# Kernel optimization log

Hardware: AMD Instinct MI355X
Metric: run time of the kernel (lower is better)

The kernel has to match this reference:

```python
import jax, jax.numpy as jnp
import numpy as np

S, B, D_MODEL, H, DH = 2048, 2, 1024, 16, 64
FACTOR = 1.0 / np.sqrt(DH).astype(np.float32)


def setup_inputs() -> dict:
    key = jax.random.key(0)
    ks = jax.random.split(key, 12)
    sc = 0.02
    inp = {
        'query': jax.random.normal(ks[0], (S, B, D_MODEL), jnp.float32),
        'key': jax.random.normal(ks[1], (S, B, D_MODEL), jnp.float32),
        'value': jax.random.normal(ks[2], (S, B, D_MODEL), jnp.float32),
        # causal mask [seq_q, seq_k, 1]; 0 -> masked
        'mask': jnp.tril(jnp.ones((S, S), dtype=bool))[:, :, None],
        'Wq': jax.random.normal(ks[3], (H * DH, D_MODEL), jnp.float32) * sc,
        'bq': jnp.zeros((H * DH,), jnp.float32),
        'Wk': jax.random.normal(ks[4], (H * DH, D_MODEL), jnp.float32) * sc,
        'bk': jnp.zeros((H * DH,), jnp.float32),
        'Wv': jax.random.normal(ks[5], (H * DH, D_MODEL), jnp.float32) * sc,
        'bv': jnp.zeros((H * DH,), jnp.float32),
        'Wo': jax.random.normal(ks[6], (D_MODEL, H * DH), jnp.float32) * sc,
        'bo': jnp.zeros((D_MODEL,), jnp.float32),
    }
    return inp


def _split_heads(x):
    # pattern: 's b (head_dim head_num) -> s b head_num head_dim' (head_dim is OUTER)
    s, b, _ = x.shape
    return x.reshape(s, b, DH, H).transpose(0, 1, 3, 2)  # [s,b,H,DH]


def reference(query, key, value, mask, Wq, bq, Wk, bk, Wv, bv, Wo, bo):
    q = _split_heads(query @ Wq.T + bq)
    k = _split_heads(key @ Wk.T + bk)
    v = _split_heads(value @ Wv.T + bv)
    scores = jnp.einsum('ibhd,jbhd->ijbh', q, k) * FACTOR  # [i,j,b,h]
    scores = jnp.where(mask[..., None], scores, -jnp.inf)
    attn = jax.nn.softmax(scores, axis=1)  # softmax over keys (dim=1)
    out = jnp.einsum('ijbh,jbhd->ibhd', attn, v)  # [i,b,h,d]
    out = out.reshape(S, B, H * DH)  # 'i b h d -> i b (h d)'
    return out @ Wo.T + bo
```

## Files before the change

kernel.cpp:

```cpp
#include <hip/hip_runtime.h>


typedef float f32x4 __attribute__((ext_vector_type(4)));
typedef float f32x16 __attribute__((ext_vector_type(16)));
typedef __bf16 bf16x8_t __attribute__((ext_vector_type(8)));
typedef unsigned short ushort8 __attribute__((ext_vector_type(8)));
typedef unsigned int uint4v __attribute__((ext_vector_type(4)));
typedef unsigned int uint2v __attribute__((ext_vector_type(2)));

#define S_LEN 2048
#define BATCH 2
#define DMODEL 1024
#define NHEAD 16
#define DHEAD 64
#define K_SCALE 0.18033688011112042f
#define NCHUNK 51

__device__ __forceinline__ unsigned short f2bf(float x) {
  unsigned int u = __builtin_bit_cast(unsigned int, x);
  u += 0x7fffu + ((u >> 16) & 1u);
  return (unsigned short)(u >> 16);
}

__device__ __forceinline__ f32x4 mfma16(ushort8 a, ushort8 b, f32x4 c) {
  return __builtin_amdgcn_mfma_f32_16x16x32_bf16(
      __builtin_bit_cast(bf16x8_t, a), __builtin_bit_cast(bf16x8_t, b), c, 0, 0, 0);
}
__device__ __forceinline__ f32x16 mfma32(ushort8 a, ushort8 b, f32x16 c) {
  return __builtin_amdgcn_mfma_f32_32x32x16_bf16(
      __builtin_bit_cast(bf16x8_t, a), __builtin_bit_cast(bf16x8_t, b), c, 0, 0, 0);
}

__device__ __forceinline__ float max3f(float a, float b, float c) {
  return fmaxf(fmaxf(a, b), c);
}

__device__ __forceinline__ ushort8 pack8(float4 a, float4 b, float s) {
  ushort8 t;
  t[0] = f2bf(a.x * s); t[1] = f2bf(a.y * s); t[2] = f2bf(a.z * s); t[3] = f2bf(a.w * s);
  t[4] = f2bf(b.x * s); t[5] = f2bf(b.y * s); t[6] = f2bf(b.z * s); t[7] = f2bf(b.w * s);
  return t;
}

__device__ __forceinline__ void gload16(unsigned short* lds, const unsigned short* g) {
  __builtin_amdgcn_global_load_lds(
      (const __attribute__((address_space(1))) unsigned int*)g,
      (__attribute__((address_space(3))) unsigned int*)lds, 16, 0, 0);
}

__global__ __launch_bounds__(256) void cvt_kernel(
    const float* __restrict__ q, const float* __restrict__ k, const float* __restrict__ v,
    const float* __restrict__ wq, const float* __restrict__ wk,
    const float* __restrict__ wv, const float* __restrict__ wo,
    unsigned short* __restrict__ qB, unsigned short* __restrict__ kB,
    unsigned short* __restrict__ vB, unsigned short* __restrict__ wqB,
    unsigned short* __restrict__ wkB, unsigned short* __restrict__ wvB,
    unsigned short* __restrict__ woB)
{
  const int c = blockIdx.x * 256 + threadIdx.x;
  const float* s; unsigned short* d; int base;
  if      (c < 524288)  { s = q;  d = qB;  base = 0; }
  else if (c < 1048576) { s = k;  d = kB;  base = 524288; }
  else if (c < 1572864) { s = v;  d = vB;  base = 1048576; }
  else if (c < 1703936) { s = wq; d = wqB; base = 1572864; }
  else if (c < 1835008) { s = wk; d = wkB; base = 1703936; }
  else if (c < 1966080) { s = wv; d = wvB; base = 1835008; }
  else                  { s = wo; d = woB; base = 1966080; }
  const size_t off = (size_t)(c - base) * 8;
  const float4 v0 = *reinterpret_cast<const float4*>(s + off);
  const float4 v1 = *reinterpret_cast<const float4*>(s + off + 4);
  *reinterpret_cast<ushort8*>(d + off) = pack8(v0, v1, 1.0f);
}

__global__ __launch_bounds__(256) void gemm_qkv_kernel(
    const unsigned short* __restrict__ qA, const unsigned short* __restrict__ kA,
    const unsigned short* __restrict__ vA,
    const unsigned short* __restrict__ wqW, const unsigned short* __restrict__ wkW,
    const unsigned short* __restrict__ wvW,
    const float* __restrict__ bq, const float* __restrict__ bk,
    const float* __restrict__ bv,
    unsigned short* __restrict__ Cq, unsigned short* __restrict__ Ck,
    unsigned short* __restrict__ Cv)
{
  __shared__ __align__(16) unsigned short As[2][128 * 64];
  __shared__ __align__(16) unsigned short Ws[2][64 * 64];
  const int z = blockIdx.z;
  const unsigned short* A = (z == 0) ? qA : (z == 1) ? kA : vA;
  const unsigned short* W = (z == 0) ? wqW : (z == 1) ? wkW : wvW;
  const float* bias = (z == 0) ? bq : (z == 1) ? bk : bv;
  unsigned short* C = (z == 0) ? Cq : (z == 1) ? Ck : Cv;
  const float oscale = (z == 1) ? K_SCALE : 1.0f;

  const int tid = threadIdx.x;
  const int lane = tid & 63;
  const int w = tid >> 6;
  const int wm = (w >> 1) * 64, wn = (w & 1) * 32;
  const int g = lane >> 4, lr = lane & 15;

  const int bid = (int)blockIdx.x;
  const int widx = (bid & 7) * 64 + (bid >> 3);
  const int n0 = (widx & 15) * 64;
  const int m0 = (widx >> 4) * 128;

  f32x4 acc[4][2] = {};

#define STAGE(buf, k0)                                                              \
  {                                                                                 \
    _Pragma("unroll")                                                               \
    for (int ii = 0; ii < 4; ++ii) {                                                \
      const int c = ii * 256 + tid;                                                 \
      const int row = c >> 3;                                                       \
      const int sl = (c & 7) ^ (row & 7);                                           \
      gload16(&As[buf][c * 8], A + (size_t)(m0 + row) * DMODEL + (k0) + sl * 8);    \
    }                                                                               \
    _Pragma("unroll")                                                               \
    for (int ii = 0; ii < 2; ++ii) {                                                \
      const int c = ii * 256 + tid;                                                 \
      const int row = c >> 3;                                                       \
      const int sl = (c & 7) ^ (row & 7);                                           \
      gload16(&Ws[buf][c * 8], W + (size_t)(n0 + row) * DMODEL + (k0) + sl * 8);    \
    }                                                                               \
  }

  STAGE(0, 0);
  int cur = 0;

  for (int t = 0; t < 16; ++t) {
    __syncthreads();
    if (t < 15) STAGE(cur ^ 1, (t + 1) * 64);

    const char* ab = (const char*)&As[cur][0];
    const char* wb = (const char*)&Ws[cur][0];
#pragma unroll
    for (int kk = 0; kk < 2; ++kk) {
      ushort8 af[4], bw[2];
#pragma unroll
      for (int mt = 0; mt < 4; ++mt) {
        const int row = wm + mt * 16 + lr;
        af[mt] = *reinterpret_cast<const ushort8*>(
            ab + row * 128 + (((kk * 4 + g) ^ (row & 7)) << 4));
      }
#pragma unroll
      for (int nt = 0; nt < 2; ++nt) {
        const int row = wn + nt * 16 + lr;
        bw[nt] = *reinterpret_cast<const ushort8*>(
            wb + row * 128 + (((kk * 4 + g) ^ (row & 7)) << 4));
      }
      __builtin_amdgcn_s_setprio(1);
#pragma unroll
      for (int mt = 0; mt < 4; ++mt)
#pragma unroll
        for (int nt = 0; nt < 2; ++nt)
          acc[mt][nt] = mfma16(af[mt], bw[nt], acc[mt][nt]);
      __builtin_amdgcn_s_setprio(0);
    }
    cur ^= 1;
  }
#undef STAGE

#pragma unroll
  for (int nt = 0; nt < 2; ++nt) {
    const int col = n0 + wn + nt * 16 + lr;
    const float bvv = bias[col];
#pragma unroll
    for (int mt = 0; mt < 4; ++mt)
#pragma unroll
      for (int r = 0; r < 4; ++r) {
        const int rowg = m0 + wm + mt * 16 + g * 4 + r;
        C[(size_t)rowg * DMODEL + col] = f2bf((acc[mt][nt][r] + bvv) * oscale);
      }
  }
}

__global__ __launch_bounds__(256) void gemm_out_kernel(
    const unsigned short* __restrict__ A, const unsigned short* __restrict__ W,
    const float* __restrict__ bias, float* __restrict__ C)
{
  __shared__ __align__(16) unsigned short As[2][128 * 64];
  __shared__ __align__(16) unsigned short Ws[2][64 * 64];
  const int tid = threadIdx.x;
  const int lane = tid & 63;
  const int w = tid >> 6;
  const int wm = (w >> 1) * 64, wn = (w & 1) * 32;
  const int g = lane >> 4, lr = lane & 15;

  const int bid = (int)blockIdx.x;
  const int widx = (bid & 7) * 64 + (bid >> 3);
  const int n0 = (widx & 15) * 64;
  const int m0 = (widx >> 4) * 128;

  f32x4 acc[4][2] = {};

#define STAGE(buf, k0)                                                              \
  {                                                                                 \
    _Pragma("unroll")                                                               \
    for (int ii = 0; ii < 4; ++ii) {                                                \
      const int c = ii * 256 + tid;                                                 \
      const int row = c >> 3;                                                       \
      const int sl = (c & 7) ^ (row & 7);                                           \
      gload16(&As[buf][c * 8], A + (size_t)(m0 + row) * DMODEL + (k0) + sl * 8);    \
    }                                                                               \
    _Pragma("unroll")                                                               \
    for (int ii = 0; ii < 2; ++ii) {                                                \
      const int c = ii * 256 + tid;                                                 \
      const int row = c >> 3;                                                       \
      const int sl = (c & 7) ^ (row & 7);                                           \
      gload16(&Ws[buf][c * 8], W + (size_t)(n0 + row) * DMODEL + (k0) + sl * 8);    \
    }                                                                               \
  }

  STAGE(0, 0);
  int cur = 0;

  for (int t = 0; t < 16; ++t) {
    __syncthreads();
    if (t < 15) STAGE(cur ^ 1, (t + 1) * 64);

    const char* ab = (const char*)&As[cur][0];
    const char* wb = (const char*)&Ws[cur][0];
#pragma unroll
    for (int kk = 0; kk < 2; ++kk) {
      ushort8 af[4], bw[2];
#pragma unroll
      for (int mt = 0; mt < 4; ++mt) {
        const int row = wm + mt * 16 + lr;
        af[mt] = *reinterpret_cast<const ushort8*>(
            ab + row * 128 + (((kk * 4 + g) ^ (row & 7)) << 4));
      }
#pragma unroll
      for (int nt = 0; nt < 2; ++nt) {
        const int row = wn + nt * 16 + lr;
        bw[nt] = *reinterpret_cast<const ushort8*>(
            wb + row * 128 + (((kk * 4 + g) ^ (row & 7)) << 4));
      }
      __builtin_amdgcn_s_setprio(1);
#pragma unroll
      for (int mt = 0; mt < 4; ++mt)
#pragma unroll
        for (int nt = 0; nt < 2; ++nt)
          acc[mt][nt] = mfma16(af[mt], bw[nt], acc[mt][nt]);
      __builtin_amdgcn_s_setprio(0);
    }
    cur ^= 1;
  }
#undef STAGE

#pragma unroll
  for (int nt = 0; nt < 2; ++nt) {
    const int col = n0 + wn + nt * 16 + lr;
    const float bvv = bias[col];
#pragma unroll
    for (int mt = 0; mt < 4; ++mt)
#pragma unroll
      for (int r = 0; r < 4; ++r) {
        const int rowg = m0 + wm + mt * 16 + g * 4 + r;
        C[(size_t)rowg * DMODEL + col] = acc[mt][nt][r] + bvv;
      }
  }
}

__global__ __launch_bounds__(256) void transpose_all_kernel(
    const unsigned short* __restrict__ in0, unsigned short* __restrict__ out0,
    const unsigned short* __restrict__ in1, unsigned short* __restrict__ out1,
    const unsigned short* __restrict__ in2, unsigned short* __restrict__ out2)
{
  __shared__ __align__(16) unsigned short T[32 * 256];
  const int bx = (int)blockIdx.x;
  const int tid = threadIdx.x;

  if (bx < 1024) {
    const unsigned short* in = (bx < 512) ? in0 : in1;
    unsigned short* out = (bx < 512) ? out0 : out1;
    const int lb = bx & 511;
    const int n0 = (lb & 127) * 32, o0 = (lb >> 7) * 256;
#pragma unroll
    for (int i = 0; i < 4; ++i) {
      const int c = i * 256 + tid;
      const int row = c >> 5, c8 = c & 31;
      ushort8 v = *reinterpret_cast<const ushort8*>(in + (size_t)(n0 + row) * DMODEL + o0 + c8 * 8);
      int y = (row * 512 + c8 * 16) ^ ((row & 3) << 5);
      *reinterpret_cast<ushort8*>((char*)T + y) = v;
    }
    __syncthreads();
    const int d0 = o0 >> 4, s0 = n0 >> 1;
#pragma unroll
    for (int rep = 0; rep < 2; ++rep) {
      const int e = rep * 256 + tid;
      const int hh = e & 15, s = (e >> 4) & 15, b = (e >> 8) & 1;
      const int n = s * 2 + b;
      unsigned short vals[16];
#pragma unroll
      for (int dd = 0; dd < 16; ++dd) {
        int y = n * 512 + ((dd * 32 + hh * 2) ^ ((n & 3) << 5));
        vals[dd] = *(const unsigned short*)((const char*)T + y);
      }
      uint4v w0, w1;
#pragma unroll
      for (int j = 0; j < 4; ++j) {
        w0[j] = (unsigned)vals[2 * j] | ((unsigned)vals[2 * j + 1] << 16);
        w1[j] = (unsigned)vals[8 + 2 * j] | ((unsigned)vals[8 + 2 * j + 1] << 16);
      }
      unsigned short* dst = out + ((size_t)(b * 16 + hh) * S_LEN + s0 + s) * DHEAD + d0;
      *reinterpret_cast<uint4v*>(dst) = w0;
      *reinterpret_cast<uint4v*>(dst + 8) = w1;
    }
  } else {
    const int lb = bx - 1024;
    const int n0 = (lb & 63) * 64, o0 = (lb >> 6) * 64;
#pragma unroll
    for (int i = 0; i < 2; ++i) {
      const int c = i * 256 + tid;
      const int row = c >> 3, c8 = c & 7;
      ushort8 v = *reinterpret_cast<const ushort8*>(in2 + (size_t)(n0 + row) * DMODEL + o0 + c8 * 8);
      int y = (row * 128 + c8 * 16) ^ ((row & 7) << 4);
      *reinterpret_cast<ushort8*>((char*)T + y) = v;
    }
    __syncthreads();
    const int d0 = o0 >> 4, s0 = n0 >> 1;
    const int shalf = tid & 1, seg = tid >> 1;
    const int dd = seg & 3, hh = (seg >> 2) & 15, b = (seg >> 6) & 1;
    unsigned short vals[16];
#pragma unroll
    for (int i = 0; i < 16; ++i) {
      const int s = shalf * 16 + i;
      const int n = s * 2 + b;
      int y = n * 128 + (((dd * 16 + hh) * 2) ^ ((n & 7) << 4));
      vals[i] = *(const unsigned short*)((const char*)T + y);
    }
    uint4v w0, w1;
#pragma unroll
    for (int j = 0; j < 4; ++j) {
      w0[j] = (unsigned)vals[2 * j] | ((unsigned)vals[2 * j + 1] << 16);
      w1[j] = (unsigned)vals[8 + 2 * j] | ((unsigned)vals[8 + 2 * j + 1] << 16);
    }
    unsigned short* dst = out2 + ((size_t)(b * 16 + hh) * DHEAD + d0 + dd) * S_LEN + s0 + shalf * 16;
    *reinterpret_cast<uint4v*>(dst) = w0;
    *reinterpret_cast<uint4v*>(dst + 8) = w1;
  }
}

__global__ __launch_bounds__(256, 4) void attn_part_kernel(
    const unsigned short* __restrict__ Qh, const unsigned short* __restrict__ Kh,
    const unsigned short* __restrict__ Vh, unsigned short* __restrict__ Opart,
    float* __restrict__ mlbuf)
{
  __shared__ __align__(16) unsigned short Ks[2][64 * 64];
  __shared__ __align__(16) unsigned short Vs[2][64 * 64];

  const int tid = threadIdx.x;
  const int lane = tid & 63;
  const int w = tid >> 6;
  const int ln31 = lane & 31;
  const int hf = lane >> 5;

  const int bid = (int)blockIdx.x;
  const int xcd = bid & 7;
  const int sl8 = bid >> 3;
  const int hb = xcd * 4 + sl8 / NCHUNK;
  const int chunkid = sl8 % NCHUNK;

  int u = chunkid;
  int Q = 0, nc = 1;
  while (u >= nc) { u -= nc; ++Q; nc = Q / 3 + 1; }
  const int c = u;

  const int head = hb & 15, b = hb >> 4;
  const int slot = hb * NCHUNK + chunkid;
  const int t0 = c * 6;
  const int tmax = 2 * Q + 1;
  const int t1 = (tmax < t0 + 5) ? tmax : (t0 + 5);
  const int q0 = Q * 128;

  const size_t hoff = (size_t)(b * NHEAD + head) * (S_LEN * DHEAD);
  const unsigned short* Qg = Qh + hoff;
  const unsigned short* Kg = Kh + hoff;
  const unsigned short* Vg = Vh + hoff;

  const int qwb = q0 + w * 32;
  const int qg = qwb + ln31;

  ushort8 qf[4];
#pragma unroll
  for (int kt = 0; kt < 4; ++kt)
    qf[kt] = *reinterpret_cast<const ushort8*>(Qg + (size_t)qg * DHEAD + kt * 16 + hf * 8);

  f32x16 oa0 = {0}, oa1 = {0};
  float mrun = -1e30f, ssum = 0.f;

#define STAGE(buf, kv)                                                             \
  {                                                                                \
    _Pragma("unroll")                                                              \
    for (int ii = 0; ii < 2; ++ii) {                                               \
      const int c2 = ii * 256 + tid;                                               \
      const int row = c2 >> 3;                                                     \
      const int sl = (c2 & 7) ^ (row & 7);                                         \
      gload16(&Ks[buf][c2 * 8], Kg + (size_t)((kv) + row) * 64 + sl * 8);          \
    }                                                                              \
    _Pragma("unroll")                                                              \
    for (int ii = 0; ii < 2; ++ii) {                                               \
      const int c2 = ii * 256 + tid;                                               \
      const int row = c2 >> 3;                                                     \
      const int sl = (c2 & 7) ^ (row & 7);                                         \
      gload16(&Vs[buf][c2 * 8], Vg + (size_t)row * S_LEN + (kv) + sl * 8);         \
    }                                                                              \
  }

  STAGE(0, t0 * 64);
  int cur = 0;

  const int kb0 = ln31 * 128 + ((hf * 16) ^ ((ln31 & 7) << 4));
  const int kb1 = (32 + ln31) * 128 + ((hf * 16) ^ ((ln31 & 7) << 4));

  for (int t = t0; t <= t1; ++t) {
    const int kv0 = t * 64;
    __syncthreads();
    if (t < t1) STAGE(cur ^ 1, kv0 + 64);

    if (kv0 <= qwb + 31) {
      f32x16 sc0 = {0}, sc1 = {0};
      {
        const char* ksb = (const char*)&Ks[cur][0];
        __builtin_amdgcn_s_setprio(1);
#pragma unroll
        for (int kt = 0; kt < 4; ++kt) {
          ushort8 kf0 = *reinterpret_cast<const ushort8*>(ksb + (kb0 ^ (kt << 5)));
          ushort8 kf1 = *reinterpret_cast<const ushort8*>(ksb + (kb1 ^ (kt << 5)));
          sc0 = mfma32(kf0, qf[kt], sc0);
          sc1 = mfma32(kf1, qf[kt], sc1);
        }
        __builtin_amdgcn_s_setprio(0);
      }

      if (kv0 + 63 > qwb) {
#pragma unroll
        for (int r = 0; r < 16; ++r) {
          const int keyb = kv0 + (r & 3) + 8 * (r >> 2) + 4 * hf;
          if (keyb > qg) sc0[r] = -1e30f;
          if (keyb + 32 > qg) sc1[r] = -1e30f;
        }
      }

      float m0a = max3f(sc0[0], sc0[1], sc0[2]);
      float m1a = max3f(sc0[3], sc0[4], sc0[5]);
      float m2a = max3f(sc0[6], sc0[7], sc0[8]);
      float m3a = max3f(sc0[9], sc0[10], sc0[11]);
      float m4a = max3f(sc0[12], sc0[13], sc0[14]);
      float m5a = max3f(sc0[15], sc1[0], sc1[1]);
      float m6a = max3f(sc1[2], sc1[3], sc1[4]);
      float m7a = max3f(sc1[5], sc1[6], sc1[7]);
      float m8a = max3f(sc1[8], sc1[9], sc1[10]);
      float m9a = max3f(sc1[11], sc1[12], sc1[13]);
      float mAa = fmaxf(sc1[14], sc1[15]);
      float n0a = max3f(m0a, m1a, m2a);
      float n1a = max3f(m3a, m4a, m5a);
      float n2a = max3f(m6a, m7a, m8a);
      float n3a = fmaxf(m9a, mAa);
      float pmax = fmaxf(max3f(n0a, n1a, n2a), n3a);
      pmax = fmaxf(pmax, __shfl_xor(pmax, 32, 64));

      if (!__all(pmax <= mrun + 8.0f)) {
        const float mnew = fmaxf(mrun, pmax);
        const float scl = exp2f(mrun - mnew);
        ssum *= scl;
#pragma unroll
        for (int r = 0; r < 16; ++r) { oa0[r] *= scl; oa1[r] *= scl; }
        mrun = mnew;
      }

      float pv0[16], pv1[16];
#pragma unroll
      for (int r = 0; r < 16; ++r) {
        pv0[r] = exp2f(sc0[r] - mrun);
        pv1[r] = exp2f(sc1[r] - mrun);
      }
      float a8[8];
#pragma unroll
      for (int r = 0; r < 8; ++r)
        a8[r] = (pv0[r] + pv0[r + 8]) + (pv1[r] + pv1[r + 8]);
      float a4_0 = a8[0] + a8[4], a4_1 = a8[1] + a8[5];
      float a4_2 = a8[2] + a8[6], a4_3 = a8[3] + a8[7];
      float psum = (a4_0 + a4_1) + (a4_2 + a4_3);
      psum += __shfl_xor(psum, 32, 64);
      ssum += psum;

      unsigned int cc[16];
#pragma unroll
      for (int j = 0; j < 8; ++j) {
        asm("v_cvt_pk_bf16_f32 %0, %1, %2" : "=v"(cc[j]) : "v"(pv0[2 * j]), "v"(pv0[2 * j + 1]));
        asm("v_cvt_pk_bf16_f32 %0, %1, %2" : "=v"(cc[8 + j]) : "v"(pv1[2 * j]), "v"(pv1[2 * j + 1]));
      }

      uint4v pfw[4];
#pragma unroll
      for (int mt = 0; mt < 2; ++mt) {
#pragma unroll
        for (int ktl = 0; ktl < 2; ++ktl) {
          const int o = mt * 8 + ktl * 4;
          unsigned x0 = cc[o + 0], x2 = cc[o + 2];
          unsigned y0 = cc[o + 1], y2 = cc[o + 3];
          asm("v_permlane32_swap_b32 %0, %1" : "+v"(x0), "+v"(x2));
          asm("v_permlane32_swap_b32 %0, %1" : "+v"(y0), "+v"(y2));
          uint4v u4;
          u4[0] = x0; u4[1] = y0; u4[2] = x2; u4[3] = y2;
          pfw[mt * 2 + ktl] = u4;
        }
      }

      {
        const char* vsb = (const char*)&Vs[cur][0];
        __builtin_amdgcn_s_setprio(1);
#pragma unroll
        for (int kt = 0; kt < 4; ++kt) {
          ushort8 vf0 = *reinterpret_cast<const ushort8*>(vsb + (kb0 ^ (kt << 5)));
          ushort8 vf1 = *reinterpret_cast<const ushort8*>(vsb + (kb1 ^ (kt << 5)));
          ushort8 pfr = __builtin_bit_cast(ushort8, pfw[kt]);
          oa0 = mfma32(vf0, pfr, oa0);
          oa1 = mfma32(vf1, pfr, oa1);
        }
        __builtin_amdgcn_s_setprio(0);
      }
    }

    cur ^= 1;
  }
#undef STAGE

  const int ql = w * 32 + ln31;
  unsigned short* ob = Opart + (size_t)slot * 8192 + ql * 64;
#pragma unroll
  for (int mt2 = 0; mt2 < 2; ++mt2) {
#pragma unroll
    for (int rq = 0; rq < 4; ++rq) {
      const int dd = mt2 * 32 + 8 * rq + 4 * hf;
      const f32x16& a = mt2 ? oa1 : oa0;
      unsigned int w0, w1;
      asm("v_cvt_pk_bf16_f32 %0, %1, %2" : "=v"(w0)
          : "v"(a[4 * rq + 0]), "v"(a[4 * rq + 1]));
      asm("v_cvt_pk_bf16_f32 %0, %1, %2" : "=v"(w1)
          : "v"(a[4 * rq + 2]), "v"(a[4 * rq + 3]));
      uint2v pk = { w0, w1 };
      *reinterpret_cast<uint2v*>(ob + dd) = pk;
    }
  }
  if (hf == 0) {
    mlbuf[slot * 256 + ql] = mrun;
    mlbuf[slot * 256 + 128 + ql] = ssum;
  }
}

__global__ __launch_bounds__(256) void attn_combine_kernel(
    const unsigned short* __restrict__ Opart, const float* __restrict__ mlbuf,
    unsigned short* __restrict__ O)
{
  const int Q = blockIdx.x, hb = blockIdx.y;
  const int head = hb & 15, b = hb >> 4;
  const int nch = Q / 3 + 1;
  int off = 0;
  for (int j = 0; j < Q; ++j) off += j / 3 + 1;
  const int s0 = hb * NCHUNK + off;

  const int tid = threadIdx.x;
  const int q = tid >> 1, dh = (tid & 1) * 32;

  float mc[6], lc[6];
  float M = -1e30f;
  for (int cc = 0; cc < nch; ++cc) {
    mc[cc] = mlbuf[(s0 + cc) * 256 + q];
    lc[cc] = mlbuf[(s0 + cc) * 256 + 128 + q];
    M = fmaxf(M, mc[cc]);
  }
  float L = 0.f, wgt[6];
  for (int cc = 0; cc < nch; ++cc) {
    wgt[cc] = exp2f(mc[cc] - M);
    L += wgt[cc] * lc[cc];
  }
  const float invL = 1.0f / L;

  float acc[32] = {};
  for (int cc = 0; cc < nch; ++cc) {
    const unsigned short* p = Opart + (size_t)(s0 + cc) * 8192 + q * 64 + dh;
    const float wv = wgt[cc];
#pragma unroll
    for (int seg = 0; seg < 4; ++seg) {
      ushort8 v = *reinterpret_cast<const ushort8*>(p + seg * 8);
#pragma unroll
      for (int j = 0; j < 8; ++j) {
        const float f = __builtin_bit_cast(float, ((unsigned int)v[j]) << 16);
        acc[seg * 8 + j] += wv * f;
      }
    }
  }

  unsigned int wpk[16];
#pragma unroll
  for (int j = 0; j < 16; ++j) {
    asm("v_cvt_pk_bf16_f32 %0, %1, %2" : "=v"(wpk[j])
        : "v"(acc[2 * j] * invL), "v"(acc[2 * j + 1] * invL));
  }
  unsigned short* dst = O + ((size_t)((Q * 128 + q) * BATCH + b)) * DMODEL + head * DHEAD + dh;
#pragma unroll
  for (int seg = 0; seg < 4; ++seg)
    *reinterpret_cast<uint4v*>(dst + seg * 8) =
        uint4v{ wpk[4 * seg], wpk[4 * seg + 1], wpk[4 * seg + 2], wpk[4 * seg + 3] };
}

extern "C" void kernel_launch(void* const* d_in, const int* in_sizes, int n_in,
                              void* d_out, int out_size, void* d_ws, size_t ws_size,
                              hipStream_t stream)
{
  (void)in_sizes; (void)n_in; (void)out_size; (void)ws_size;
  const float* query = (const float*)d_in[0];
  const float* key_  = (const float*)d_in[1];
  const float* value = (const float*)d_in[2];
  const float* Wq = (const float*)d_in[4];
  const float* bq = (const float*)d_in[5];
  const float* Wk = (const float*)d_in[6];
  const float* bk = (const float*)d_in[7];
  const float* Wv = (const float*)d_in[8];
  const float* bv = (const float*)d_in[9];
  const float* Wo = (const float*)d_in[10];
  const float* bo = (const float*)d_in[11];
  float* out = (float*)d_out;

  const size_t NE = (size_t)4096 * DMODEL;
  const size_t NW = (size_t)DMODEL * DMODEL;
  unsigned short* qB  = (unsigned short*)d_ws;
  unsigned short* kB  = qB + NE;
  unsigned short* vB  = kB + NE;
  unsigned short* g1  = vB + NE;
  unsigned short* Qh  = g1 + NE;
  unsigned short* Kh  = Qh + NE;
  unsigned short* Vh  = Kh + NE;
  unsigned short* wqB = Vh + NE;
  unsigned short* wkB = wqB + NW;
  unsigned short* wvB = wkB + NW;
  unsigned short* woB = wvB + NW;
  unsigned short* Opart = vB;
  float* mlbuf = (float*)(Opart + (size_t)(NCHUNK * 32) * 8192);

  cvt_kernel<<<dim3(8192), 256, 0, stream>>>(query, key_, value, Wq, Wk, Wv, Wo,
                                             qB, kB, vB, wqB, wkB, wvB, woB);
  gemm_qkv_kernel<<<dim3(512, 1, 3), 256, 0, stream>>>(
      qB, kB, vB, wqB, wkB, wvB, bq, bk, bv, g1, Qh, Kh);
  transpose_all_kernel<<<dim3(2048), 256, 0, stream>>>(g1, qB, Qh, Vh, Kh, kB);
  attn_part_kernel<<<dim3(NCHUNK * 32), 256, 0, stream>>>(qB, Vh, kB, Opart, mlbuf);
  attn_combine_kernel<<<dim3(16, 32), 256, 0, stream>>>(Opart, mlbuf, qB);
  gemm_out_kernel<<<dim3(512), 256, 0, stream>>>(qB, woB, bo, out);
}
```

Measured before the change: 134.2 us.

## Fuse fp32-to-bf16 activation conversion into QKV GEMM A-tile staging

```diff
diff --git a/kernel.cpp b/kernel.cpp
--- a/kernel.cpp
+++ b/kernel.cpp
@@ -42,6 +42,15 @@
   return t;
 }
 
+__device__ __forceinline__ uint4v pack8_pk(const f32x4& a, const f32x4& b) {
+  uint4v r;
+  asm("v_cvt_pk_bf16_f32 %0, %1, %2" : "=v"(r[0]) : "v"(a[0]), "v"(a[1]));
+  asm("v_cvt_pk_bf16_f32 %0, %1, %2" : "=v"(r[1]) : "v"(a[2]), "v"(a[3]));
+  asm("v_cvt_pk_bf16_f32 %0, %1, %2" : "=v"(r[2]) : "v"(b[0]), "v"(b[1]));
+  asm("v_cvt_pk_bf16_f32 %0, %1, %2" : "=v"(r[3]) : "v"(b[2]), "v"(b[3]));
+  return r;
+}
+
 __device__ __forceinline__ void gload16(unsigned short* lds, const unsigned short* g) {
   __builtin_amdgcn_global_load_lds(
       (const __attribute__((address_space(1))) unsigned int*)g,
@@ -49,23 +58,17 @@
 }
 
 __global__ __launch_bounds__(256) void cvt_kernel(
-    const float* __restrict__ q, const float* __restrict__ k, const float* __restrict__ v,
     const float* __restrict__ wq, const float* __restrict__ wk,
     const float* __restrict__ wv, const float* __restrict__ wo,
-    unsigned short* __restrict__ qB, unsigned short* __restrict__ kB,
-    unsigned short* __restrict__ vB, unsigned short* __restrict__ wqB,
-    unsigned short* __restrict__ wkB, unsigned short* __restrict__ wvB,
-    unsigned short* __restrict__ woB)
+    unsigned short* __restrict__ wqB, unsigned short* __restrict__ wkB,
+    unsigned short* __restrict__ wvB, unsigned short* __restrict__ woB)
 {
   const int c = blockIdx.x * 256 + threadIdx.x;
   const float* s; unsigned short* d; int base;
-  if      (c < 524288)  { s = q;  d = qB;  base = 0; }
-  else if (c < 1048576) { s = k;  d = kB;  base = 524288; }
-  else if (c < 1572864) { s = v;  d = vB;  base = 1048576; }
-  else if (c < 1703936) { s = wq; d = wqB; base = 1572864; }
-  else if (c < 1835008) { s = wk; d = wkB; base = 1703936; }
-  else if (c < 1966080) { s = wv; d = wvB; base = 1835008; }
-  else                  { s = wo; d = woB; base = 1966080; }
+  if      (c < 131072) { s = wq; d = wqB; base = 0; }
+  else if (c < 262144) { s = wk; d = wkB; base = 131072; }
+  else if (c < 393216) { s = wv; d = wvB; base = 262144; }
+  else                 { s = wo; d = woB; base = 393216; }
   const size_t off = (size_t)(c - base) * 8;
   const float4 v0 = *reinterpret_cast<const float4*>(s + off);
   const float4 v1 = *reinterpret_cast<const float4*>(s + off + 4);
@@ -73,8 +76,8 @@
 }
 
 __global__ __launch_bounds__(256) void gemm_qkv_kernel(
-    const unsigned short* __restrict__ qA, const unsigned short* __restrict__ kA,
-    const unsigned short* __restrict__ vA,
+    const float* __restrict__ qA, const float* __restrict__ kA,
+    const float* __restrict__ vA,
     const unsigned short* __restrict__ wqW, const unsigned short* __restrict__ wkW,
     const unsigned short* __restrict__ wvW,
     const float* __restrict__ bq, const float* __restrict__ bk,
@@ -85,7 +88,7 @@
   __shared__ __align__(16) unsigned short As[2][128 * 64];
   __shared__ __align__(16) unsigned short Ws[2][64 * 64];
   const int z = blockIdx.z;
-  const unsigned short* A = (z == 0) ? qA : (z == 1) ? kA : vA;
+  const float* A = (z == 0) ? qA : (z == 1) ? kA : vA;
   const unsigned short* W = (z == 0) ? wqW : (z == 1) ? wkW : wvW;
   const float* bias = (z == 0) ? bq : (z == 1) ? bk : bv;
   unsigned short* C = (z == 0) ? Cq : (z == 1) ? Ck : Cv;
@@ -102,17 +105,36 @@
   const int n0 = (widx & 15) * 64;
   const int m0 = (widx >> 4) * 128;
 
-  f32x4 acc[4][2] = {};
-
-#define STAGE(buf, k0)                                                              \
+  const int ar0 = tid >> 3, asl = tid & 7;
+  const float* abase = A + (size_t)(m0 + ar0) * DMODEL + asl * 8;
+  int adst[4];
+#pragma unroll
+  for (int ii = 0; ii < 4; ++ii) {
+    const int row = ar0 + ii * 32;
+    adst[ii] = row * 128 + ((asl ^ (row & 7)) << 4);
+  }
+
+  f32x4 sa[4][2];
+
+#define LOADA(k0)                                                                   \
   {                                                                                 \
     _Pragma("unroll")                                                               \
     for (int ii = 0; ii < 4; ++ii) {                                                \
-      const int c = ii * 256 + tid;                                                 \
-      const int row = c >> 3;                                                       \
-      const int sl = (c & 7) ^ (row & 7);                                           \
-      gload16(&As[buf][c * 8], A + (size_t)(m0 + row) * DMODEL + (k0) + sl * 8);    \
+      const float* p = abase + (size_t)(ii * 32) * DMODEL + (k0);                   \
+      sa[ii][0] = *reinterpret_cast<const f32x4*>(p);                               \
+      sa[ii][1] = *reinterpret_cast<const f32x4*>(p + 4);                           \
     }                                                                               \
+  }
+#define WRITEA(buf)                                                                 \
+  {                                                                                 \
+    _Pragma("unroll")                                                               \
+    for (int ii = 0; ii < 4; ++ii) {                                                \
+      uint4v pk = pack8_pk(sa[ii][0], sa[ii][1]);                                   \
+      *reinterpret_cast<uint4v*>((char*)&As[buf][0] + adst[ii]) = pk;               \
+    }                                                                               \
+  }
+#define STAGEW(buf, k0)                                                             \
+  {                                                                                 \
     _Pragma("unroll")                                                               \
     for (int ii = 0; ii < 2; ++ii) {                                                \
       const int c = ii * 256 + tid;                                                 \
@@ -122,12 +144,19 @@
     }                                                                               \
   }
 
-  STAGE(0, 0);
+  f32x4 acc[4][2] = {};
+
+  LOADA(0);
+  STAGEW(0, 0);
+  WRITEA(0);
   int cur = 0;
 
   for (int t = 0; t < 16; ++t) {
     __syncthreads();
-    if (t < 15) STAGE(cur ^ 1, (t + 1) * 64);
+
+    const int kn = (t < 15 ? t + 1 : 15) * 64;
+    LOADA(kn);
+    if (t < 15) STAGEW(cur ^ 1, kn);
 
     const char* ab = (const char*)&As[cur][0];
     const char* wb = (const char*)&Ws[cur][0];
@@ -154,9 +183,13 @@
           acc[mt][nt] = mfma16(af[mt], bw[nt], acc[mt][nt]);
       __builtin_amdgcn_s_setprio(0);
     }
+
+    WRITEA(cur ^ 1);
     cur ^= 1;
   }
-#undef STAGE
+#undef LOADA
+#undef WRITEA
+#undef STAGEW
 
 #pragma unroll
   for (int nt = 0; nt < 2; ++nt) {
@@ -638,10 +671,9 @@
   unsigned short* Opart = vB;
   float* mlbuf = (float*)(Opart + (size_t)(NCHUNK * 32) * 8192);
 
-  cvt_kernel<<<dim3(8192), 256, 0, stream>>>(query, key_, value, Wq, Wk, Wv, Wo,
-                                             qB, kB, vB, wqB, wkB, wvB, woB);
+  cvt_kernel<<<dim3(2048), 256, 0, stream>>>(Wq, Wk, Wv, Wo, wqB, wkB, wvB, woB);
   gemm_qkv_kernel<<<dim3(512, 1, 3), 256, 0, stream>>>(
-      qB, kB, vB, wqB, wkB, wvB, bq, bk, bv, g1, Qh, Kh);
+      query, key_, value, wqB, wkB, wvB, bq, bk, bv, g1, Qh, Kh);
   transpose_all_kernel<<<dim3(2048), 256, 0, stream>>>(g1, qB, Qh, Vh, Kh, kB);
   attn_part_kernel<<<dim3(NCHUNK * 32), 256, 0, stream>>>(qB, Vh, kB, Opart, mlbuf);
   attn_combine_kernel<<<dim3(16, 32), 256, 0, stream>>>(Opart, mlbuf, qB);
```

Measured after the change: 142.1 us. 5.9% more time.

## Fuse head-split transpose into QKV GEMM epilogue and drop transpose kernel

Applied to the files above, without the earlier changes.

```diff
diff --git a/kernel.cpp b/kernel.cpp
--- a/kernel.cpp
+++ b/kernel.cpp
@@ -158,6 +158,8 @@
   }
 #undef STAGE
 
+  __syncthreads();
+  unsigned short* T = &As[0][0];
 #pragma unroll
   for (int nt = 0; nt < 2; ++nt) {
     const int col = n0 + wn + nt * 16 + lr;
@@ -166,9 +168,50 @@
     for (int mt = 0; mt < 4; ++mt)
 #pragma unroll
       for (int r = 0; r < 4; ++r) {
-        const int rowg = m0 + wm + mt * 16 + g * 4 + r;
-        C[(size_t)rowg * DMODEL + col] = f2bf((acc[mt][nt][r] + bvv) * oscale);
-      }
+        const int lrow = wm + mt * 16 + g * 4 + r;
+        T[lrow * 64 + wn + nt * 16 + lr] = f2bf((acc[mt][nt][r] + bvv) * oscale);
+      }
+  }
+  __syncthreads();
+
+  const int dfirst = n0 >> 4;
+  if (z < 2) {
+#pragma unroll
+    for (int it = 0; it < 8; ++it) {
+      const int e = it * 256 + tid;
+      const int h = e & 15, lrow = e >> 4;
+      const int n = m0 + lrow, s = n >> 1, bb = n & 1;
+      const unsigned short v0 = T[lrow * 64 + 0 * 16 + h];
+      const unsigned short v1 = T[lrow * 64 + 1 * 16 + h];
+      const unsigned short v2 = T[lrow * 64 + 2 * 16 + h];
+      const unsigned short v3 = T[lrow * 64 + 3 * 16 + h];
+      uint2v pk = { (unsigned)v0 | ((unsigned)v1 << 16),
+                    (unsigned)v2 | ((unsigned)v3 << 16) };
+      *reinterpret_cast<uint2v*>(
+          C + ((size_t)(bb * 16 + h) * S_LEN + s) * DHEAD + dfirst) = pk;
+    }
+  } else {
+    const int run = tid >> 1, shalf = tid & 1;
+    const int bb = run >> 6, rem = run & 63;
+    const int h = rem >> 2, dl = rem & 3;
+    const int sbase = (m0 >> 1) + shalf * 32;
+    unsigned short vals[32];
+#pragma unroll
+    for (int i = 0; i < 32; ++i) {
+      const int lrow = (shalf * 32 + i) * 2 + bb;
+      vals[i] = T[lrow * 64 + dl * 16 + h];
+    }
+    unsigned short* dstp =
+        C + ((size_t)(bb * 16 + h) * DHEAD + dfirst + dl) * S_LEN + sbase;
+#pragma unroll
+    for (int seg = 0; seg < 4; ++seg) {
+      uint4v pk;
+#pragma unroll
+      for (int j = 0; j < 4; ++j)
+        pk[j] = (unsigned)vals[seg * 8 + 2 * j] |
+                ((unsigned)vals[seg * 8 + 2 * j + 1] << 16);
+      *reinterpret_cast<uint4v*>(dstp + seg * 8) = pk;
+    }
   }
 }
 
@@ -256,86 +299,6 @@
         const int rowg = m0 + wm + mt * 16 + g * 4 + r;
         C[(size_t)rowg * DMODEL + col] = acc[mt][nt][r] + bvv;
       }
-  }
-}
-
-__global__ __launch_bounds__(256) void transpose_all_kernel(
-    const unsigned short* __restrict__ in0, unsigned short* __restrict__ out0,
-    const unsigned short* __restrict__ in1, unsigned short* __restrict__ out1,
-    const unsigned short* __restrict__ in2, unsigned short* __restrict__ out2)
-{
-  __shared__ __align__(16) unsigned short T[32 * 256];
-  const int bx = (int)blockIdx.x;
-  const int tid = threadIdx.x;
-
-  if (bx < 1024) {
-    const unsigned short* in = (bx < 512) ? in0 : in1;
-    unsigned short* out = (bx < 512) ? out0 : out1;
-    const int lb = bx & 511;
-    const int n0 = (lb & 127) * 32, o0 = (lb >> 7) * 256;
-#pragma unroll
-    for (int i = 0; i < 4; ++i) {
-      const int c = i * 256 + tid;
-      const int row = c >> 5, c8 = c & 31;
-      ushort8 v = *reinterpret_cast<const ushort8*>(in + (size_t)(n0 + row) * DMODEL + o0 + c8 * 8);
-      int y = (row * 512 + c8 * 16) ^ ((row & 3) << 5);
-      *reinterpret_cast<ushort8*>((char*)T + y) = v;
-    }
-    __syncthreads();
-    const int d0 = o0 >> 4, s0 = n0 >> 1;
-#pragma unroll
-    for (int rep = 0; rep < 2; ++rep) {
-      const int e = rep * 256 + tid;
-      const int hh = e & 15, s = (e >> 4) & 15, b = (e >> 8) & 1;
-      const int n = s * 2 + b;
-      unsigned short vals[16];
-#pragma unroll
-      for (int dd = 0; dd < 16; ++dd) {
-        int y = n * 512 + ((dd * 32 + hh * 2) ^ ((n & 3) << 5));
-        vals[dd] = *(const unsigned short*)((const char*)T + y);
-      }
-      uint4v w0, w1;
-#pragma unroll
-      for (int j = 0; j < 4; ++j) {
-        w0[j] = (unsigned)vals[2 * j] | ((unsigned)vals[2 * j + 1] << 16);
-        w1[j] = (unsigned)vals[8 + 2 * j] | ((unsigned)vals[8 + 2 * j + 1] << 16);
-      }
-      unsigned short* dst = out + ((size_t)(b * 16 + hh) * S_LEN + s0 + s) * DHEAD + d0;
-      *reinterpret_cast<uint4v*>(dst) = w0;
-      *reinterpret_cast<uint4v*>(dst + 8) = w1;
-    }
-  } else {
-    const int lb = bx - 1024;
-    const int n0 = (lb & 63) * 64, o0 = (lb >> 6) * 64;
-#pragma unroll
-    for (int i = 0; i < 2; ++i) {
-      const int c = i * 256 + tid;
-      const int row = c >> 3, c8 = c & 7;
-      ushort8 v = *reinterpret_cast<const ushort8*>(in2 + (size_t)(n0 + row) * DMODEL + o0 + c8 * 8);
-      int y = (row * 128 + c8 * 16) ^ ((row & 7) << 4);
-      *reinterpret_cast<ushort8*>((char*)T + y) = v;
-    }
-    __syncthreads();
-    const int d0 = o0 >> 4, s0 = n0 >> 1;
-    const int shalf = tid & 1, seg = tid >> 1;
-    const int dd = seg & 3, hh = (seg >> 2) & 15, b = (seg >> 6) & 1;
-    unsigned short vals[16];
-#pragma unroll
-    for (int i = 0; i < 16; ++i) {
-      const int s = shalf * 16 + i;
-      const int n = s * 2 + b;
-      int y = n * 128 + (((dd * 16 + hh) * 2) ^ ((n & 7) << 4));
-      vals[i] = *(const unsigned short*)((const char*)T + y);
-    }
-    uint4v w0, w1;
-#pragma unroll
-    for (int j = 0; j < 4; ++j) {
-      w0[j] = (unsigned)vals[2 * j] | ((unsigned)vals[2 * j + 1] << 16);
-      w1[j] = (unsigned)vals[8 + 2 * j] | ((unsigned)vals[8 + 2 * j + 1] << 16);
-    }
-    unsigned short* dst = out2 + ((size_t)(b * 16 + hh) * DHEAD + d0 + dd) * S_LEN + s0 + shalf * 16;
-    *reinterpret_cast<uint4v*>(dst) = w0;
-    *reinterpret_cast<uint4v*>(dst + 8) = w1;
   }
 }
 
@@ -628,22 +591,21 @@
   unsigned short* kB  = qB + NE;
   unsigned short* vB  = kB + NE;
   unsigned short* g1  = vB + NE;
-  unsigned short* Qh  = g1 + NE;
-  unsigned short* Kh  = Qh + NE;
-  unsigned short* Vh  = Kh + NE;
-  unsigned short* wqB = Vh + NE;
+  unsigned short* Qhm = g1 + NE;
+  unsigned short* Khm = Qhm + NE;
+  unsigned short* Vdm = Khm + NE;
+  unsigned short* wqB = Vdm + NE;
   unsigned short* wkB = wqB + NW;
   unsigned short* wvB = wkB + NW;
   unsigned short* woB = wvB + NW;
-  unsigned short* Opart = vB;
+  unsigned short* Opart = qB;
   float* mlbuf = (float*)(Opart + (size_t)(NCHUNK * 32) * 8192);
 
   cvt_kernel<<<dim3(8192), 256, 0, stream>>>(query, key_, value, Wq, Wk, Wv, Wo,
                                              qB, kB, vB, wqB, wkB, wvB, woB);
   gemm_qkv_kernel<<<dim3(512, 1, 3), 256, 0, stream>>>(
-      qB, kB, vB, wqB, wkB, wvB, bq, bk, bv, g1, Qh, Kh);
-  transpose_all_kernel<<<dim3(2048), 256, 0, stream>>>(g1, qB, Qh, Vh, Kh, kB);
-  attn_part_kernel<<<dim3(NCHUNK * 32), 256, 0, stream>>>(qB, Vh, kB, Opart, mlbuf);
-  attn_combine_kernel<<<dim3(16, 32), 256, 0, stream>>>(Opart, mlbuf, qB);
-  gemm_out_kernel<<<dim3(512), 256, 0, stream>>>(qB, woB, bo, out);
-}
+      qB, kB, vB, wqB, wkB, wvB, bq, bk, bv, Qhm, Khm, Vdm);
+  attn_part_kernel<<<dim3(NCHUNK * 32), 256, 0, stream>>>(Qhm, Khm, Vdm, Opart, mlbuf);
+  attn_combine_kernel<<<dim3(16, 32), 256, 0, stream>>>(Opart, mlbuf, Qhm);
+  gemm_out_kernel<<<dim3(512), 256, 0, stream>>>(Qhm, woB, bo, out);
+}
```

Result: no change. 135.6 us (+1.0%).
